# Performance work log

Measured on AMD Instinct MI355X. Metric: run time of the kernel, lower is better.

Reference implementation:

```python
import jax, jax.numpy as jnp
import numpy as np

B, H, W = 2, 240, 1216
CH_G = 64
K_F = 3
PAD_F = 1            # (k_f-1)//2
K_G = 3
PAD_G = 1            # (k_g-1)//2
NUM = K_F * K_F - 1  # 8 nonlocal neighbors
IDX_REF = NUM // 2   # 4
PROP_TIME = 18
GAMMA = 0.5


def _bilinear(f, ys, xs):
    """Zero-padded bilinear sampling. f: (B,H,W); ys,xs: (B,K,H,W) -> (B,K,H,W)."""
    Hf, Wf = f.shape[-2], f.shape[-1]
    y0 = jnp.floor(ys)
    x0 = jnp.floor(xs)
    wy1 = ys - y0
    wx1 = xs - x0
    gather = jax.vmap(lambda fb, yy, xx: fb[yy, xx])  # over batch

    def corner(yi, xi, w):
        valid = ((yi >= 0) & (yi < Hf) & (xi >= 0) & (xi < Wf)).astype(f.dtype)
        yc = jnp.clip(yi, 0, Hf - 1).astype(jnp.int32)
        xc = jnp.clip(xi, 0, Wf - 1).astype(jnp.int32)
        return w * valid * gather(f, yc, xc)

    return (corner(y0, x0, (1 - wy1) * (1 - wx1))
            + corner(y0, x0 + 1, (1 - wy1) * wx1)
            + corner(y0 + 1, x0, wy1 * (1 - wx1))
            + corner(y0 + 1, x0 + 1, wy1 * wx1))


def _forward(feat_init, guidance, confidence, feat_fix, w_oa, b_oa, aff_scale):
    Bn, _, Hn, Wn = guidance.shape
    dt = feat_init.dtype

    # guidance -> offsets + raw affinities (3*NUM channels)
    oa = jax.lax.conv_general_dilated(
        guidance, w_oa, (1, 1), ((PAD_G, PAD_G), (PAD_G, PAD_G)),
        dimension_numbers=('NCHW', 'OIHW', 'NCHW')) + b_oa[None, :, None, None]
    o1, o2, aff = oa[:, :NUM], oa[:, NUM:2 * NUM], oa[:, 2 * NUM:]
    # same channel reinterpretation as torch: cat(o1,o2).view(B,NUM,2,H,W)
    offset = jnp.concatenate([o1, o2], axis=1).reshape(Bn, NUM, 2, Hn, Wn)

    # TGASS affinity scaling
    aff = jnp.tanh(aff) / (aff_scale[0] + 1e-8)

    hh = jnp.arange(Hn, dtype=dt)[:, None]   # (H,1)
    ww = jnp.arange(Wn, dtype=dt)[None, :]   # (1,W)

    # confidence propagation: 1x1 deform conv at each nonlocal offset (offsets detached)
    off_ng = jax.lax.stop_gradient(offset)
    ys_c = hh + off_ng[:, :, 0]  # (B,NUM,H,W)
    xs_c = ww + off_ng[:, :, 1]
    conf_aff = _bilinear(confidence[:, 0], ys_c, xs_c)
    aff = aff * conf_aff

    # normalize (ASS/TGASS style clamp)
    aff_abs_sum = jnp.maximum(jnp.sum(jnp.abs(aff), axis=1, keepdims=True) + 1e-4, 1.0)
    aff = aff / aff_abs_sum
    aff_ref = 1.0 - jnp.sum(aff, axis=1, keepdims=True)
    aff_full = jnp.concatenate([aff[:, :IDX_REF], aff_ref, aff[:, IDX_REF:]], axis=1)  # (B,9,H,W)

    zeros_ref = jnp.zeros((Bn, 1, 2, Hn, Wn), dt)
    offset_full = jnp.concatenate([offset[:, :IDX_REF], zeros_ref, offset[:, IDX_REF:]], axis=1)

    # sampling grid for the 3x3 deformable propagation (w = ones, b = 0)
    k = jnp.arange(K_F * K_F)
    kh = (k // K_F - PAD_F).astype(dt)[None, :, None, None]
    kw = (k % K_F - PAD_F).astype(dt)[None, :, None, None]
    ys = hh + kh + offset_full[:, :, 0]  # (B,9,H,W)
    xs = ww + kw + offset_full[:, :, 1]

    mask_fix = (jnp.sum((feat_fix > 0.0).astype(dt), axis=1, keepdims=True) > 0.0).astype(dt)

    def step(feat, _):
        feat = (1.0 - mask_fix) * feat + mask_fix * feat_fix
        samp = _bilinear(feat[:, 0], ys, xs)                    # (B,9,H,W)
        feat = jnp.sum(aff_full * samp, axis=1, keepdims=True)  # (B,1,H,W)
        return feat, None

    feat_result, _ = jax.lax.scan(step, feat_init, None, length=PROP_TIME)
    return feat_result, offset_full.reshape(Bn, -1, Hn, Wn), aff_full


def setup_inputs() -> dict:
    key = jax.random.key(0)
    k1, k2, k3, k4, k5, k6 = jax.random.split(key, 6)
    feat_init = jax.random.normal(k1, (B, 1, H, W), jnp.float32)
    guidance = jax.random.normal(k2, (B, CH_G, H, W), jnp.float32)
    confidence = jax.random.uniform(k3, (B, 1, H, W), jnp.float32)
    sparse = (jax.random.uniform(k4, (B, 1, H, W)) < 0.05).astype(jnp.float32)
    feat_fix = jax.random.uniform(k5, (B, 1, H, W), jnp.float32, 1.0, 80.0) * sparse
    w_oa = jax.random.normal(k6, (3 * NUM, CH_G, K_G, K_G), jnp.float32) * 0.01
    b_oa = jnp.zeros((3 * NUM,), jnp.float32)
    aff_scale = jnp.full((1,), GAMMA * NUM, jnp.float32)
    return {"feat_init": feat_init, "guidance": guidance, "confidence": confidence,
            "feat_fix": feat_fix, "w_oa": w_oa, "b_oa": b_oa, "aff_scale": aff_scale}


def reference(feat_init, guidance, confidence, feat_fix, w_oa, b_oa, aff_scale):
    return _forward(feat_init, guidance, confidence, feat_fix, w_oa, b_oa, aff_scale)
```

## Files before the change

kernel.cpp:

```cpp
#include <hip/hip_runtime.h>
#include <math.h>

#define Bc   2
#define Hc   240
#define Wc   1216
#define CHG  64
#define HWc  (Hc*Wc)
#define NPIX (Bc*HWc)

#define OUT1 (NPIX)
#define OUT2 (OUT1 + Bc*18*HWc)

__device__ __forceinline__ float bilin(const float* __restrict__ f, float ys, float xs) {
    float y0f = floorf(ys), x0f = floorf(xs);
    float wy1 = ys - y0f,   wx1 = xs - x0f;
    float wy0 = 1.f - wy1,  wx0 = 1.f - wx1;
    int y0 = (int)y0f, x0 = (int)x0f;
    int y1 = y0 + 1,   x1 = x0 + 1;
    int y0c = min(max(y0, 0), Hc-1), y1c = min(max(y1, 0), Hc-1);
    int x0c = min(max(x0, 0), Wc-1), x1c = min(max(x1, 0), Wc-1);
    float my0 = (y0 >= 0 && y0 < Hc) ? 1.f : 0.f;
    float my1 = (y1 >= 0 && y1 < Hc) ? 1.f : 0.f;
    float mx0 = (x0 >= 0 && x0 < Wc) ? 1.f : 0.f;
    float mx1 = (x1 >= 0 && x1 < Wc) ? 1.f : 0.f;
    float v00 = f[y0c*Wc + x0c] * (my0*mx0);
    float v01 = f[y0c*Wc + x1c] * (my0*mx1);
    float v10 = f[y1c*Wc + x0c] * (my1*mx0);
    float v11 = f[y1c*Wc + x1c] * (my1*mx1);
    return wy0*(wx0*v00 + wx1*v01) + wy1*(wx0*v10 + wx1*v11);
}

__global__ void reorder_w(const float* __restrict__ w_oa, float* __restrict__ wr) {
    int i = blockIdx.x*256 + threadIdx.x;
    if (i < 24*576) {
        int oc = i / 576; int cj = i - oc*576;
        wr[cj*24 + oc] = w_oa[i];
    }
}

__global__ __launch_bounds__(256) void conv_epilogue(
    const float* __restrict__ guid, const float* __restrict__ conf,
    const float* __restrict__ wr,   const float* __restrict__ b_oa,
    const float* __restrict__ aff_scale,
    const float* __restrict__ feat_init, const float* __restrict__ feat_fix,
    float* __restrict__ dout, float* __restrict__ buf0)
{
    int p  = blockIdx.x*256 + threadIdx.x;
    int b  = p / HWc;
    int hw = p - b*HWc;
    int h  = hw / Wc;
    int w  = hw - h*Wc;

    int   aoff[9];
    float msk[9];
    #pragma unroll
    for (int dy = 0; dy < 3; ++dy) {
        int hy = h + dy - 1;
        float my = (hy >= 0 && hy < Hc) ? 1.f : 0.f;
        int hyc = min(max(hy, 0), Hc-1);
        #pragma unroll
        for (int dx = 0; dx < 3; ++dx) {
            int wx = w + dx - 1;
            float mx = (wx >= 0 && wx < Wc) ? 1.f : 0.f;
            int wxc = min(max(wx, 0), Wc-1);
            aoff[dy*3+dx] = hyc*Wc + wxc;
            msk [dy*3+dx] = my*mx;
        }
    }

    float acc[24];
    #pragma unroll
    for (int oc = 0; oc < 24; ++oc) acc[oc] = b_oa[oc];

    const float* gb = guid + b*CHG*HWc;
    for (int c = 0; c < CHG; ++c) {
        const float* gc = gb + c*HWc;
        #pragma unroll
        for (int j = 0; j < 9; ++j) {
            float g = gc[aoff[j]] * msk[j];
            const float* wp = wr + (c*9 + j)*24;
            #pragma unroll
            for (int oc = 0; oc < 24; ++oc)
                acc[oc] = fmaf(g, wp[oc], acc[oc]);
        }
    }

    float scale = 1.f / (aff_scale[0] + 1e-8f);
    const float* cb = conf + b*HWc;
    float oyv[8], oxv[8], af[8];
    float ssum = 0.f;
    #pragma unroll
    for (int k = 0; k < 8; ++k) { oyv[k] = acc[2*k]; oxv[k] = acc[2*k+1]; }
    #pragma unroll
    for (int k = 0; k < 8; ++k) {
        float a  = tanhf(acc[16+k]) * scale;
        float ys = (float)h + oyv[k];
        float xs = (float)w + oxv[k];
        float ca = bilin(cb, ys, xs);
        a *= ca;
        af[k] = a;
        ssum += fabsf(a);
    }
    float inv = 1.f / fmaxf(ssum + 1e-4f, 1.f);
    float asum = 0.f;
    #pragma unroll
    for (int k = 0; k < 8; ++k) { af[k] *= inv; asum += af[k]; }
    float aref = 1.f - asum;

    float* ob = dout + OUT1 + b*18*HWc + hw;
    float* ab = dout + OUT2 + b*9*HWc  + hw;
    #pragma unroll
    for (int kf = 0; kf < 9; ++kf) {
        float oy, ox, av;
        if (kf == 4) { oy = 0.f; ox = 0.f; av = aref; }
        else { int k = (kf < 4) ? kf : kf-1; oy = oyv[k]; ox = oxv[k]; av = af[k]; }
        ob[(2*kf  )*HWc] = oy;
        ob[(2*kf+1)*HWc] = ox;
        ab[kf*HWc]       = av;
    }

    float ff = feat_fix[p];
    buf0[p] = (ff > 0.f) ? ff : feat_init[p];
}

__global__ __launch_bounds__(256) void prop_step(
    const float* __restrict__ fin,
    const float* __restrict__ doff,
    const float* __restrict__ daff,
    const float* __restrict__ feat_fix,
    float* __restrict__ out, int apply_mask)
{
    int p  = blockIdx.x*256 + threadIdx.x;
    int b  = p / HWc;
    int hw = p - b*HWc;
    int h  = hw / Wc;
    int w  = hw - h*Wc;

    const float* fb = fin  + b*HWc;
    const float* ob = doff + b*18*HWc + hw;
    const float* ab = daff + b*9*HWc  + hw;

    float s = 0.f;
    #pragma unroll
    for (int kf = 0; kf < 9; ++kf) {
        float offy = ob[(2*kf  )*HWc];
        float offx = ob[(2*kf+1)*HWc];
        float a    = ab[kf*HWc];
        float ys = (float)(h + kf/3 - 1) + offy;
        float xs = (float)(w + kf%3 - 1) + offx;
        s += a * bilin(fb, ys, xs);
    }
    if (apply_mask) {
        float ff = feat_fix[p];
        out[p] = (ff > 0.f) ? ff : s;
    } else {
        out[p] = s;
    }
}

extern "C" void kernel_launch(void* const* d_in, const int* in_sizes, int n_in,
                              void* d_out, int out_size, void* d_ws, size_t ws_size,
                              hipStream_t stream) {
    const float* feat_init  = (const float*)d_in[0];
    const float* guidance   = (const float*)d_in[1];
    const float* confidence = (const float*)d_in[2];
    const float* feat_fix   = (const float*)d_in[3];
    const float* w_oa       = (const float*)d_in[4];
    const float* b_oa       = (const float*)d_in[5];
    const float* aff_scale  = (const float*)d_in[6];
    float* out = (float*)d_out;

    float* wr   = (float*)d_ws;
    float* buf0 = wr + 24*576;
    float* buf1 = buf0 + NPIX;

    reorder_w<<<(24*576 + 255)/256, 256, 0, stream>>>(w_oa, wr);
    conv_epilogue<<<NPIX/256, 256, 0, stream>>>(
        guidance, confidence, wr, b_oa, aff_scale, feat_init, feat_fix, out, buf0);

    float* doff = out + OUT1;
    float* daff = out + OUT2;
    float* bufs[2] = {buf0, buf1};
    for (int i = 1; i <= 18; ++i) {
        const float* fi = bufs[(i-1) & 1];
        float* fo = (i == 18) ? out : bufs[i & 1];
        prop_step<<<NPIX/256, 256, 0, stream>>>(fi, doff, daff, feat_fix, fo, (i < 18) ? 1 : 0);
    }
}
```

Before: 711.9 us.

## Pack offsets/affinities to bf16 for propagation and register-block conv over four pixels

Result: slower. 1.199 ms (+68.4%).

```diff
diff --git a/kernel.cpp b/kernel.cpp
--- a/kernel.cpp
+++ b/kernel.cpp
@@ -10,6 +10,21 @@
 
 #define OUT1 (NPIX)
 #define OUT2 (OUT1 + Bc*18*HWc)
+
+#define WS_WR    0
+#define WS_BUF0  (13824)
+#define WS_BUF1  (WS_BUF0 + NPIX)
+#define WS_OFFPK (WS_BUF1 + NPIX)
+#define WS_AFFPK (WS_OFFPK + 8*NPIX)
+
+__device__ __forceinline__ unsigned short f2bf(float x) {
+    unsigned u = __float_as_uint(x);
+    unsigned r = (u + 0x7fffu + ((u >> 16) & 1u)) >> 16;
+    return (unsigned short)r;
+}
+__device__ __forceinline__ float bf2f(unsigned short u) {
+    return __uint_as_float(((unsigned)u) << 16);
+}
 
 __device__ __forceinline__ float bilin(const float* __restrict__ f, float ys, float xs) {
     float y0f = floorf(ys), x0f = floorf(xs);
@@ -43,90 +58,144 @@
     const float* __restrict__ wr,   const float* __restrict__ b_oa,
     const float* __restrict__ aff_scale,
     const float* __restrict__ feat_init, const float* __restrict__ feat_fix,
-    float* __restrict__ dout, float* __restrict__ buf0)
+    float* __restrict__ dout, float* __restrict__ buf0,
+    unsigned* __restrict__ off_pk, unsigned short* __restrict__ aff_pk)
 {
-    int p  = blockIdx.x*256 + threadIdx.x;
-    int b  = p / HWc;
-    int hw = p - b*HWc;
-    int h  = hw / Wc;
-    int w  = hw - h*Wc;
-
-    int   aoff[9];
-    float msk[9];
+    int nwg = gridDim.x;
+    int q = nwg >> 3, r = nwg & 7;
+    int xcd = blockIdx.x & 7, pos = blockIdx.x >> 3;
+    int sb = (xcd < r ? xcd*(q+1) : r*(q+1) + (xcd - r)*q) + pos;
+
+    int gp = sb*256 + threadIdx.x;
+    int b   = gp / (HWc/4);
+    int rem = gp - b*(HWc/4);
+    int h   = rem / (Wc/4);
+    int wq  = rem - h*(Wc/4);
+    int w0  = wq * 4;
+
+    int   rowoff[3]; bool okY[3];
     #pragma unroll
     for (int dy = 0; dy < 3; ++dy) {
         int hy = h + dy - 1;
-        float my = (hy >= 0 && hy < Hc) ? 1.f : 0.f;
-        int hyc = min(max(hy, 0), Hc-1);
-        #pragma unroll
-        for (int dx = 0; dx < 3; ++dx) {
-            int wx = w + dx - 1;
-            float mx = (wx >= 0 && wx < Wc) ? 1.f : 0.f;
-            int wxc = min(max(wx, 0), Wc-1);
-            aoff[dy*3+dx] = hyc*Wc + wxc;
-            msk [dy*3+dx] = my*mx;
-        }
-    }
-
-    float acc[24];
-    #pragma unroll
-    for (int oc = 0; oc < 24; ++oc) acc[oc] = b_oa[oc];
-
-    const float* gb = guid + b*CHG*HWc;
+        okY[dy]   = (hy >= 0) & (hy < Hc);
+        rowoff[3-1-(2-dy)] = min(max(hy, 0), Hc-1) * Wc;
+    }
+    bool lok = (wq > 0);
+    bool rok = (wq < (Wc/4 - 1));
+
+    float acc[24][4];
+    #pragma unroll
+    for (int oc = 0; oc < 24; ++oc) {
+        float bv = b_oa[oc];
+        #pragma unroll
+        for (int px = 0; px < 4; ++px) acc[oc][px] = bv;
+    }
+
+    const float* gb = guid + (size_t)b*CHG*HWc;
     for (int c = 0; c < CHG; ++c) {
         const float* gc = gb + c*HWc;
-        #pragma unroll
-        for (int j = 0; j < 9; ++j) {
-            float g = gc[aoff[j]] * msk[j];
-            const float* wp = wr + (c*9 + j)*24;
+        const float* wcp = wr + c*216;
+        #pragma unroll
+        for (int dy = 0; dy < 3; ++dy) {
+            const float* rp = gc + rowoff[dy];
+            float V[6];
+            if (okY[dy]) {
+                float4 vm = *(const float4*)(rp + w0);
+                V[0] = lok ? rp[w0-1] : 0.f;
+                V[1] = vm.x; V[2] = vm.y; V[3] = vm.z; V[4] = vm.w;
+                V[5] = rok ? rp[w0+4] : 0.f;
+            } else {
+                #pragma unroll
+                for (int i = 0; i < 6; ++i) V[i] = 0.f;
+            }
             #pragma unroll
-            for (int oc = 0; oc < 24; ++oc)
-                acc[oc] = fmaf(g, wp[oc], acc[oc]);
+            for (int dx = 0; dx < 3; ++dx) {
+                const float* wj = wcp + (dy*3+dx)*24;
+                #pragma unroll
+                for (int oc = 0; oc < 24; ++oc) {
+                    float wv = wj[oc];
+                    acc[oc][0] = fmaf(V[dx+0], wv, acc[oc][0]);
+                    acc[oc][1] = fmaf(V[dx+1], wv, acc[oc][1]);
+                    acc[oc][2] = fmaf(V[dx+2], wv, acc[oc][2]);
+                    acc[oc][3] = fmaf(V[dx+3], wv, acc[oc][3]);
+                }
+            }
         }
     }
 
     float scale = 1.f / (aff_scale[0] + 1e-8f);
-    const float* cb = conf + b*HWc;
-    float oyv[8], oxv[8], af[8];
-    float ssum = 0.f;
-    #pragma unroll
-    for (int k = 0; k < 8; ++k) { oyv[k] = acc[2*k]; oxv[k] = acc[2*k+1]; }
+    const float* cb = conf + (size_t)b*HWc;
+    float af[8][4], aref[4];
+    #pragma unroll
+    for (int px = 0; px < 4; ++px) {
+        float av[8]; float ssum = 0.f;
+        #pragma unroll
+        for (int k = 0; k < 8; ++k) {
+            float a  = tanhf(acc[16+k][px]) * scale;
+            float ys = (float)h        + acc[2*k  ][px];
+            float xs = (float)(w0+px)  + acc[2*k+1][px];
+            a *= bilin(cb, ys, xs);
+            av[k] = a; ssum += fabsf(a);
+        }
+        float inv = 1.f / fmaxf(ssum + 1e-4f, 1.f);
+        float s2 = 0.f;
+        #pragma unroll
+        for (int k = 0; k < 8; ++k) { av[k] *= inv; s2 += av[k]; af[k][px] = av[k]; }
+        aref[px] = 1.f - s2;
+    }
+
+    int hw0 = h*Wc + w0;
+    float* ob = dout + OUT1 + (size_t)b*18*HWc + hw0;
+    float* ab = dout + OUT2 + (size_t)b*9*HWc  + hw0;
+    #pragma unroll
+    for (int kf = 0; kf < 9; ++kf) {
+        float4 vy, vx, va;
+        if (kf == 4) {
+            vy = make_float4(0.f,0.f,0.f,0.f);
+            vx = make_float4(0.f,0.f,0.f,0.f);
+            va = make_float4(aref[0], aref[1], aref[2], aref[3]);
+        } else {
+            int k = (kf < 4) ? kf : kf-1;
+            vy = make_float4(acc[2*k  ][0], acc[2*k  ][1], acc[2*k  ][2], acc[2*k  ][3]);
+            vx = make_float4(acc[2*k+1][0], acc[2*k+1][1], acc[2*k+1][2], acc[2*k+1][3]);
+            va = make_float4(af[k][0], af[k][1], af[k][2], af[k][3]);
+        }
+        *(float4*)(ob + (size_t)(2*kf  )*HWc) = vy;
+        *(float4*)(ob + (size_t)(2*kf+1)*HWc) = vx;
+        *(float4*)(ab + (size_t)kf*HWc)       = va;
+    }
+
+    unsigned*       opk = off_pk + (size_t)(b*8)*HWc + hw0;
+    unsigned short* apk = aff_pk + (size_t)(b*8)*HWc + hw0;
     #pragma unroll
     for (int k = 0; k < 8; ++k) {
-        float a  = tanhf(acc[16+k]) * scale;
-        float ys = (float)h + oyv[k];
-        float xs = (float)w + oxv[k];
-        float ca = bilin(cb, ys, xs);
-        a *= ca;
-        af[k] = a;
-        ssum += fabsf(a);
-    }
-    float inv = 1.f / fmaxf(ssum + 1e-4f, 1.f);
-    float asum = 0.f;
-    #pragma unroll
-    for (int k = 0; k < 8; ++k) { af[k] *= inv; asum += af[k]; }
-    float aref = 1.f - asum;
-
-    float* ob = dout + OUT1 + b*18*HWc + hw;
-    float* ab = dout + OUT2 + b*9*HWc  + hw;
-    #pragma unroll
-    for (int kf = 0; kf < 9; ++kf) {
-        float oy, ox, av;
-        if (kf == 4) { oy = 0.f; ox = 0.f; av = aref; }
-        else { int k = (kf < 4) ? kf : kf-1; oy = oyv[k]; ox = oxv[k]; av = af[k]; }
-        ob[(2*kf  )*HWc] = oy;
-        ob[(2*kf+1)*HWc] = ox;
-        ab[kf*HWc]       = av;
-    }
-
-    float ff = feat_fix[p];
-    buf0[p] = (ff > 0.f) ? ff : feat_init[p];
+        uint4 pk;
+        pk.x = (unsigned)f2bf(acc[2*k][0]) | ((unsigned)f2bf(acc[2*k+1][0]) << 16);
+        pk.y = (unsigned)f2bf(acc[2*k][1]) | ((unsigned)f2bf(acc[2*k+1][1]) << 16);
+        pk.z = (unsigned)f2bf(acc[2*k][2]) | ((unsigned)f2bf(acc[2*k+1][2]) << 16);
+        pk.w = (unsigned)f2bf(acc[2*k][3]) | ((unsigned)f2bf(acc[2*k+1][3]) << 16);
+        *(uint4*)(opk + (size_t)k*HWc) = pk;
+        ushort4 aa;
+        aa.x = f2bf(af[k][0]); aa.y = f2bf(af[k][1]);
+        aa.z = f2bf(af[k][2]); aa.w = f2bf(af[k][3]);
+        *(ushort4*)(apk + (size_t)k*HWc) = aa;
+    }
+
+    int p0 = b*HWc + hw0;
+    float4 ff4 = *(const float4*)(feat_fix  + p0);
+    float4 fi4 = *(const float4*)(feat_init + p0);
+    float4 o;
+    o.x = (ff4.x > 0.f) ? ff4.x : fi4.x;
+    o.y = (ff4.y > 0.f) ? ff4.y : fi4.y;
+    o.z = (ff4.z > 0.f) ? ff4.z : fi4.z;
+    o.w = (ff4.w > 0.f) ? ff4.w : fi4.w;
+    *(float4*)(buf0 + p0) = o;
 }
 
 __global__ __launch_bounds__(256) void prop_step(
     const float* __restrict__ fin,
-    const float* __restrict__ doff,
-    const float* __restrict__ daff,
+    const unsigned* __restrict__ off_pk,
+    const unsigned short* __restrict__ aff_pk,
     const float* __restrict__ feat_fix,
     float* __restrict__ out, int apply_mask)
 {
@@ -136,20 +205,25 @@
     int h  = hw / Wc;
     int w  = hw - h*Wc;
 
-    const float* fb = fin  + b*HWc;
-    const float* ob = doff + b*18*HWc + hw;
-    const float* ab = daff + b*9*HWc  + hw;
-
-    float s = 0.f;
-    #pragma unroll
-    for (int kf = 0; kf < 9; ++kf) {
-        float offy = ob[(2*kf  )*HWc];
-        float offx = ob[(2*kf+1)*HWc];
-        float a    = ab[kf*HWc];
+    const float* fb = fin + (size_t)b*HWc;
+    const unsigned*       opk = off_pk + (size_t)(b*8)*HWc + hw;
+    const unsigned short* apk = aff_pk + (size_t)(b*8)*HWc + hw;
+
+    float s = 0.f, asum = 0.f;
+    #pragma unroll
+    for (int k = 0; k < 8; ++k) {
+        int kf = (k < 4) ? k : k+1;
+        unsigned pk = opk[(size_t)k*HWc];
+        float offy = bf2f((unsigned short)(pk & 0xffffu));
+        float offx = bf2f((unsigned short)(pk >> 16));
+        float a    = bf2f(apk[(size_t)k*HWc]);
         float ys = (float)(h + kf/3 - 1) + offy;
         float xs = (float)(w + kf%3 - 1) + offx;
         s += a * bilin(fb, ys, xs);
-    }
+        asum += a;
+    }
+    s += (1.f - asum) * fb[hw];
+
     if (apply_mask) {
         float ff = feat_fix[p];
         out[p] = (ff > 0.f) ? ff : s;
@@ -170,20 +244,22 @@
     const float* aff_scale  = (const float*)d_in[6];
     float* out = (float*)d_out;
 
-    float* wr   = (float*)d_ws;
-    float* buf0 = wr + 24*576;
-    float* buf1 = buf0 + NPIX;
+    float* wsf = (float*)d_ws;
+    float* wr   = wsf + WS_WR;
+    float* buf0 = wsf + WS_BUF0;
+    float* buf1 = wsf + WS_BUF1;
+    unsigned*       off_pk = (unsigned*)(wsf + WS_OFFPK);
+    unsigned short* aff_pk = (unsigned short*)(wsf + WS_AFFPK);
 
     reorder_w<<<(24*576 + 255)/256, 256, 0, stream>>>(w_oa, wr);
-    conv_epilogue<<<NPIX/256, 256, 0, stream>>>(
-        guidance, confidence, wr, b_oa, aff_scale, feat_init, feat_fix, out, buf0);
-
-    float* doff = out + OUT1;
-    float* daff = out + OUT2;
+    conv_epilogue<<<(NPIX/4)/256, 256, 0, stream>>>(
+        guidance, confidence, wr, b_oa, aff_scale, feat_init, feat_fix,
+        out, buf0, off_pk, aff_pk);
+
     float* bufs[2] = {buf0, buf1};
     for (int i = 1; i <= 18; ++i) {
         const float* fi = bufs[(i-1) & 1];
         float* fo = (i == 18) ? out : bufs[i & 1];
-        prop_step<<<NPIX/256, 256, 0, stream>>>(fi, doff, daff, feat_fix, fo, (i < 18) ? 1 : 0);
-    }
-}
+        prop_step<<<NPIX/256, 256, 0, stream>>>(fi, off_pk, aff_pk, feat_fix, fo, (i < 18) ? 1 : 0);
+    }
+}
```
